# Optimization experiments

Measured on AMD Instinct MI355X. Metric: run time of the kernel, lower is better.

The kernel has to match this reference:

```python
import jax, jax.numpy as jnp
import numpy as np

CIN, COUT, R, N, B = 4, 4, 4, 4096, 32

def setup_inputs() -> dict:
    key = jax.random.key(0)
    k1, k2, k3 = jax.random.split(key, 3)
    x = jax.random.normal(k1, (CIN, B, N), dtype=jnp.float32)
    # torch.nn.init.normal(std=0.01)
    G = 0.01 * jax.random.normal(k2, (CIN, COUT, R, N), dtype=jnp.float32)
    H = 0.01 * jax.random.normal(k3, (CIN, COUT, R, N), dtype=jnp.float32)
    return {"x": x, "G": G, "H": H}

def reference(x, G, H):
    """LDR layer, displacement='toep_corner' (cycle=True).

    For each channel pair (i,j):
        M_ij = sum_s C_1(G[i,j,s]) @ C_{-1}(H[i,j,s])^T
    where C_f(v) is the f-circulant matrix with first column v
    (= Krylov matrix of the f-unit-circulant shift Z_f with vector v).
    out[j] = sum_i M_ij @ x[i]^T  (batched over batch dim).

    Identities used (F = DFT):
      C_1(u) y      = ifft(fft(u) * fft(y))
      C_1(u)^T y    = fft(fft(u) * ifft(y))
      C_f(v)        = D^{-1} C_1(D v) D,  D = diag(zeta^k), zeta = f^{1/n}
      => C_{-1}(h)^T y = D * fft(fft(D*h) * ifft(conj(D)*y)), D_k = exp(i*pi*k/n)
    All channel pairs and ranks are batched in a single FFT call (no Python
    loops over channels, unlike the original double loop).
    """
    cin, b, n = x.shape
    k = jnp.arange(n)
    D = jnp.exp(1j * jnp.pi * k / n).astype(jnp.complex64)   # zeta^k for f=-1
    Dinv = jnp.conj(D)

    # --- step 1: t[i,j,s,b,:] = C_{-1}(H[i,j,s])^T x[i,b,:]  -> (cin,cout,r,b,n)
    Hf = jnp.fft.fft(D * H.astype(jnp.complex64), axis=-1)           # (cin,cout,r,n)
    Xf = jnp.fft.ifft(Dinv * x.astype(jnp.complex64), axis=-1)       # (cin,b,n)
    t = D * jnp.fft.fft(Hf[:, :, :, None, :] * Xf[:, None, None, :, :], axis=-1)

    # --- step 2: out[j,b,:] = Re ifft( sum_{i,s} fft(G[i,j,s]) * fft(t[i,j,s,b]) )
    Gf = jnp.fft.fft(G, axis=-1).astype(jnp.complex64)               # (cin,cout,r,n)
    Tf = jnp.fft.fft(t, axis=-1)                                     # (cin,cout,r,b,n)
    Yf = jnp.einsum('ijsn,ijsbn->jbn', Gf, Tf)                       # (cout,b,n)
    return jnp.real(jnp.fft.ifft(Yf, axis=-1)).astype(x.dtype)
```

## Files before the change

kernel.cpp:

```cpp
#include <hip/hip_runtime.h>
#include <math.h>


#define NFFT  4096
#define NT    256
#define CIN   4
#define COUT  4
#define RANK  4
#define BATCH 32
#define PI_F  3.14159265358979323846f

__device__ __forceinline__ float2 cmul(float2 a, float2 b) {
    return make_float2(a.x*b.x - a.y*b.y, a.x*b.y + a.y*b.x);
}
__device__ __forceinline__ float2 cadd(float2 a, float2 b){ return make_float2(a.x+b.x, a.y+b.y); }
__device__ __forceinline__ float2 csub(float2 a, float2 b){ return make_float2(a.x-b.x, a.y-b.y); }

__device__ __forceinline__ int SW(int e){ return e ^ ((e >> 4) & 15); }

template<int SIGN>
__device__ __forceinline__ void dft16(float2 v[16]) {
    const float sgn = (float)SIGN;
    const float C8 = 0.923879532511287f, S8 = 0.382683432365090f, H2 = 0.707106781186548f;
    const float2 w1 = make_float2( C8,  sgn*S8);
    const float2 w2 = make_float2( H2,  sgn*H2);
    const float2 w3 = make_float2( S8,  sgn*C8);
    const float2 w4 = make_float2(0.f,  sgn);
    const float2 w6 = make_float2(-H2,  sgn*H2);
    const float2 w9 = make_float2(-C8, -sgn*S8);
    float2 t[16];
    #pragma unroll
    for (int p = 0; p < 4; ++p) {
        float2 a0 = v[p], a1 = v[p+4], a2 = v[p+8], a3 = v[p+12];
        float2 b0 = cadd(a0,a2), b1 = csub(a0,a2), b2 = cadd(a1,a3), b3 = csub(a1,a3);
        float2 ib3 = make_float2(-sgn*b3.y, sgn*b3.x);
        float2 X0 = cadd(b0,b2), X2c = csub(b0,b2);
        float2 X1 = cadd(b1,ib3), X3 = csub(b1,ib3);
        if (p == 1) { X1 = cmul(X1,w1); X2c = cmul(X2c,w2); X3 = cmul(X3,w3); }
        else if (p == 2) { X1 = cmul(X1,w2); X2c = cmul(X2c,w4); X3 = cmul(X3,w6); }
        else if (p == 3) { X1 = cmul(X1,w3); X2c = cmul(X2c,w6); X3 = cmul(X3,w9); }
        t[4*p+0]=X0; t[4*p+1]=X1; t[4*p+2]=X2c; t[4*p+3]=X3;
    }
    #pragma unroll
    for (int q = 0; q < 4; ++q) {
        float2 a0 = t[q], a1 = t[q+4], a2 = t[q+8], a3 = t[q+12];
        float2 b0 = cadd(a0,a2), b1 = csub(a0,a2), b2 = cadd(a1,a3), b3 = csub(a1,a3);
        float2 ib3 = make_float2(-sgn*b3.y, sgn*b3.x);
        v[q+0]  = cadd(b0,b2);
        v[q+8]  = csub(b0,b2);
        v[q+4]  = cadd(b1,ib3);
        v[q+12] = csub(b1,ib3);
    }
}

__device__ __forceinline__ void twiddle16(float2 v[16], float ang) {
    float sn, cs; __sincosf(ang, &sn, &cs);
    float2 w = make_float2(cs, sn), t = w;
    v[1] = cmul(v[1], t);
    #pragma unroll
    for (int k = 2; k < 16; ++k) { t = cmul(t, w); v[k] = cmul(v[k], t); }
}

template<int SIGN>
__device__ void fft4096_r16(float2 v[16], float2* lds, int tid) {
    dft16<SIGN>(v);
    twiddle16(v, (float)SIGN * 2.0f * PI_F * (float)tid / 4096.0f);
    #pragma unroll
    for (int k = 0; k < 16; ++k) lds[SW(16*tid + k)] = v[k];
    __syncthreads();
    #pragma unroll
    for (int r = 0; r < 16; ++r) v[r] = lds[SW(tid + 256*r)];
    dft16<SIGN>(v);
    twiddle16(v, (float)SIGN * 2.0f * PI_F * (float)(tid >> 4) / 256.0f);
    __syncthreads();
    {
        const int q = tid & 15, p = tid >> 4;
        #pragma unroll
        for (int k = 0; k < 16; ++k) lds[SW(q + 256*p + 16*k)] = v[k];
    }
    __syncthreads();
    #pragma unroll
    for (int r = 0; r < 16; ++r) v[r] = lds[SW(tid + 256*r)];
    dft16<SIGN>(v);
    __syncthreads();
}

__global__ __launch_bounds__(NT, 2) void ldr_pre_k(
    const float* __restrict__ x, const float* __restrict__ G, const float* __restrict__ H,
    float2* __restrict__ Hf, float2* __restrict__ Gf, float2* __restrict__ Xf)
{
    __shared__ float2 lds[NFFT];
    const int tid = threadIdx.x;
    const int bid = blockIdx.x;
    float2 v[16];
    if (bid < 64) {
        const float* h = H + (size_t)bid * NFFT;
        float sn, cs; __sincosf(PI_F * (float)tid / (float)NFFT, &sn, &cs);
        float2 d = make_float2(cs, sn);
        const float2 dstep = make_float2(0.980785280403230449f, 0.195090322016128268f);
        #pragma unroll
        for (int k = 0; k < 16; ++k) {
            float hv = h[tid + 256*k];
            v[k] = make_float2(d.x*hv, d.y*hv);
            d = cmul(d, dstep);
        }
        fft4096_r16<-1>(v, lds, tid);
        float2* o = Hf + (size_t)bid * NFFT;
        #pragma unroll
        for (int k = 0; k < 16; ++k) o[tid + 256*k] = v[k];
    } else if (bid < 128) {
        const int row = bid - 64;
        const float* g = G + (size_t)row * NFFT;
        #pragma unroll
        for (int k = 0; k < 16; ++k) v[k] = make_float2(g[tid + 256*k], 0.0f);
        fft4096_r16<-1>(v, lds, tid);
        float2* o = Gf + (size_t)row * NFFT;
        #pragma unroll
        for (int k = 0; k < 16; ++k) o[tid + 256*k] = v[k];
    } else {
        const int row = bid - 128;
        const float* xp = x + (size_t)row * NFFT;
        float sn, cs; __sincosf(PI_F * (float)tid / (float)NFFT, &sn, &cs);
        float2 d = make_float2(cs, -sn);
        const float2 dstep = make_float2(0.980785280403230449f, -0.195090322016128268f);
        #pragma unroll
        for (int k = 0; k < 16; ++k) {
            float xv = xp[tid + 256*k];
            v[k] = make_float2(d.x*xv, d.y*xv);
            d = cmul(d, dstep);
        }
        fft4096_r16<1>(v, lds, tid);
        const float invn = 1.0f / (float)NFFT;
        float2* o = Xf + (size_t)row * NFFT;
        #pragma unroll
        for (int k = 0; k < 16; ++k) o[tid + 256*k] = make_float2(v[k].x*invn, v[k].y*invn);
    }
}

__global__ __launch_bounds__(NT, 2) void ldr_mid_k(
    const float2* __restrict__ Hf, const float2* __restrict__ Xf,
    const float2* __restrict__ Gf, float2* __restrict__ Ph)
{
    __shared__ float2 lds[NFFT];
    const int tid = threadIdx.x;
    const int bid = blockIdx.x;
    const int b   = bid & (BATCH - 1);
    const int is_ = bid >> 5;
    const int s   = is_ & 3;
    const int ij  = is_ >> 2;
    const int i   = ij >> 2;
    const int j   = ij & 3;
    const float2* xrow = Xf + (size_t)(i*BATCH + b) * NFFT;
    const float2* hrow = Hf + (size_t)is_ * NFFT;
    const float2* grow = Gf + (size_t)is_ * NFFT;

    float2 v[16];
    #pragma unroll
    for (int k = 0; k < 16; ++k) {
        const int e = tid + 256*k;
        v[k] = cmul(hrow[e], xrow[e]);
    }
    fft4096_r16<-1>(v, lds, tid);
    {
        float sn, cs; __sincosf(PI_F * (float)tid / (float)NFFT, &sn, &cs);
        float2 d = make_float2(cs, sn);
        const float2 dstep = make_float2(0.980785280403230449f, 0.195090322016128268f);
        #pragma unroll
        for (int k = 0; k < 16; ++k) { v[k] = cmul(v[k], d); d = cmul(d, dstep); }
    }
    fft4096_r16<-1>(v, lds, tid);
    const int u = i * RANK + s;
    float2* prow = Ph + (size_t)((u*COUT + j)*BATCH + b) * (NFFT/2);
    float2 y0 = cmul(grow[tid], v[0]);
    if (tid == 0) {
        const float2 ynyq = cmul(grow[2048], v[8]);
        y0 = make_float2(y0.x, ynyq.x);
    }
    prow[tid] = y0;
    #pragma unroll
    for (int k = 1; k < 8; ++k) {
        const int e = tid + 256*k;
        prow[e] = cmul(grow[e], v[k]);
    }
}

__global__ __launch_bounds__(NT, 2) void ldr_fin_k(
    const float2* __restrict__ Ph, float* __restrict__ out)
{
    __shared__ float2 lds[NFFT];
    __shared__ float2 sh[NFFT/2];
    const int tid = threadIdx.x;
    const int bid = blockIdx.x;
    const int b = bid & (BATCH - 1);
    const int j = bid >> 5;

    float2 a[8];
    #pragma unroll
    for (int k = 0; k < 8; ++k) a[k] = make_float2(0.0f, 0.0f);
    #pragma unroll
    for (int u = 0; u < 16; ++u) {
        const float2* row = Ph + (size_t)((u*COUT + j)*BATCH + b) * (NFFT/2);
        #pragma unroll
        for (int k = 0; k < 8; ++k) a[k] = cadd(a[k], row[tid + 256*k]);
    }
    #pragma unroll
    for (int k = 0; k < 8; ++k) sh[tid + 256*k] = a[k];
    __syncthreads();

    const float dc  = sh[0].x;
    const float nyq = sh[0].y;
    float2 v[16];
    #pragma unroll
    for (int k = 0; k < 8; ++k) v[k] = a[k];
    if (tid == 0) v[0] = make_float2(dc, 0.0f);
    #pragma unroll
    for (int k = 8; k < 16; ++k) {
        const int m = 4096 - (tid + 256*k);
        if (m == 2048) {
            v[k] = make_float2(nyq, 0.0f);
        } else {
            float2 c = sh[m];
            v[k] = make_float2(c.x, -c.y);
        }
    }
    fft4096_r16<1>(v, lds, tid);
    const float invn = 1.0f / (float)NFFT;
    float* orow = out + (size_t)bid * NFFT;
    #pragma unroll
    for (int k = 0; k < 16; ++k) orow[tid + 256*k] = v[k].x * invn;
}

extern "C" void kernel_launch(void* const* d_in, const int* in_sizes, int n_in,
                              void* d_out, int out_size, void* d_ws, size_t ws_size,
                              hipStream_t stream) {
    const float* x = (const float*)d_in[0];
    const float* G = (const float*)d_in[1];
    const float* H = (const float*)d_in[2];
    float* out = (float*)d_out;

    float2* Hf = (float2*)d_ws;
    float2* Gf = Hf + (size_t)64 * NFFT;
    float2* Xf = Gf + (size_t)64 * NFFT;
    float2* Ph = Xf + (size_t)128 * NFFT;

    ldr_pre_k<<<256, NT, 0, stream>>>(x, G, H, Hf, Gf, Xf);
    ldr_mid_k<<<CIN * COUT * RANK * BATCH, NT, 0, stream>>>(Hf, Xf, Gf, Ph);
    ldr_fin_k<<<COUT * BATCH, NT, 0, stream>>>(Ph, out);
}
```

Before: 108.4 us.

## Fuse rank pairs in mid kernel, prune second forward FFT outputs, vectorize reduction

The mid kernel now processes two ranks per block and accumulates their G-weighted spectra in registers, halving the Ph partial-sum buffer and the blocks launched. The second forward FFT uses a pruned final radix-16 stage that computes only the lower half of the outputs the real-output path needs. The final reduction reads half as many partial rows with float4 loads. Twiddle generation is split into odd and even chains to shorten the serial dependency. In exchange each mid block does twice the work, giving fewer blocks and less parallelism.

```diff
diff --git a/kernel.cpp b/kernel.cpp
--- a/kernel.cpp
+++ b/kernel.cpp
@@ -53,12 +53,53 @@
     }
 }
 
+template<int SIGN>
+__device__ __forceinline__ void dft16_low(float2 v[16]) {
+    const float sgn = (float)SIGN;
+    const float C8 = 0.923879532511287f, S8 = 0.382683432365090f, H2 = 0.707106781186548f;
+    const float2 w1 = make_float2( C8,  sgn*S8);
+    const float2 w2 = make_float2( H2,  sgn*H2);
+    const float2 w3 = make_float2( S8,  sgn*C8);
+    const float2 w4 = make_float2(0.f,  sgn);
+    const float2 w6 = make_float2(-H2,  sgn*H2);
+    const float2 w9 = make_float2(-C8, -sgn*S8);
+    float2 t[16];
+    #pragma unroll
+    for (int p = 0; p < 4; ++p) {
+        float2 a0 = v[p], a1 = v[p+4], a2 = v[p+8], a3 = v[p+12];
+        float2 b0 = cadd(a0,a2), b1 = csub(a0,a2), b2 = cadd(a1,a3), b3 = csub(a1,a3);
+        float2 ib3 = make_float2(-sgn*b3.y, sgn*b3.x);
+        float2 X0 = cadd(b0,b2), X2c = csub(b0,b2);
+        float2 X1 = cadd(b1,ib3), X3 = csub(b1,ib3);
+        if (p == 1) { X1 = cmul(X1,w1); X2c = cmul(X2c,w2); X3 = cmul(X3,w3); }
+        else if (p == 2) { X1 = cmul(X1,w2); X2c = cmul(X2c,w4); X3 = cmul(X3,w6); }
+        else if (p == 3) { X1 = cmul(X1,w3); X2c = cmul(X2c,w6); X3 = cmul(X3,w9); }
+        t[4*p+0]=X0; t[4*p+1]=X1; t[4*p+2]=X2c; t[4*p+3]=X3;
+    }
+    #pragma unroll
+    for (int q = 0; q < 4; ++q) {
+        float2 a0 = t[q], a1 = t[q+4], a2 = t[q+8], a3 = t[q+12];
+        float2 b0 = cadd(a0,a2), b1 = csub(a0,a2), b2 = cadd(a1,a3), b3 = csub(a1,a3);
+        float2 ib3 = make_float2(-sgn*b3.y, sgn*b3.x);
+        v[q+0]  = cadd(b0,b2);
+        v[q+4]  = cadd(b1,ib3);
+        if (q == 0) v[8] = csub(b0,b2);
+    }
+}
+
 __device__ __forceinline__ void twiddle16(float2 v[16], float ang) {
     float sn, cs; __sincosf(ang, &sn, &cs);
-    float2 w = make_float2(cs, sn), t = w;
-    v[1] = cmul(v[1], t);
-    #pragma unroll
-    for (int k = 2; k < 16; ++k) { t = cmul(t, w); v[k] = cmul(v[k], t); }
+    float2 w  = make_float2(cs, sn);
+    float2 w2 = cmul(w, w);
+    float2 to = w;
+    float2 te = w2;
+    v[1] = cmul(v[1], to);
+    v[2] = cmul(v[2], te);
+    #pragma unroll
+    for (int k = 3; k < 16; k += 2) {
+        to = cmul(to, w2); v[k] = cmul(v[k], to);
+        if (k + 1 < 16) { te = cmul(te, w2); v[k+1] = cmul(v[k+1], te); }
+    }
 }
 
 template<int SIGN>
@@ -83,6 +124,30 @@
     for (int r = 0; r < 16; ++r) v[r] = lds[SW(tid + 256*r)];
     dft16<SIGN>(v);
     __syncthreads();
+}
+
+template<bool TAIL_SYNC>
+__device__ void fft4096_fwd_low(float2 v[16], float2* lds, int tid) {
+    dft16<-1>(v);
+    twiddle16(v, -2.0f * PI_F * (float)tid / 4096.0f);
+    #pragma unroll
+    for (int k = 0; k < 16; ++k) lds[SW(16*tid + k)] = v[k];
+    __syncthreads();
+    #pragma unroll
+    for (int r = 0; r < 16; ++r) v[r] = lds[SW(tid + 256*r)];
+    dft16<-1>(v);
+    twiddle16(v, -2.0f * PI_F * (float)(tid >> 4) / 256.0f);
+    __syncthreads();
+    {
+        const int q = tid & 15, p = tid >> 4;
+        #pragma unroll
+        for (int k = 0; k < 16; ++k) lds[SW(q + 256*p + 16*k)] = v[k];
+    }
+    __syncthreads();
+    #pragma unroll
+    for (int r = 0; r < 16; ++r) v[r] = lds[SW(tid + 256*r)];
+    dft16_low<-1>(v);
+    if (TAIL_SYNC) __syncthreads();
 }
 
 __global__ __launch_bounds__(NT, 2) void ldr_pre_k(
@@ -145,43 +210,54 @@
     const int tid = threadIdx.x;
     const int bid = blockIdx.x;
     const int b   = bid & (BATCH - 1);
-    const int is_ = bid >> 5;
-    const int s   = is_ & 3;
-    const int ij  = is_ >> 2;
+    const int is2 = bid >> 5;
+    const int sg  = is2 & 1;
+    const int ij  = is2 >> 1;
     const int i   = ij >> 2;
     const int j   = ij & 3;
     const float2* xrow = Xf + (size_t)(i*BATCH + b) * NFFT;
-    const float2* hrow = Hf + (size_t)is_ * NFFT;
-    const float2* grow = Gf + (size_t)is_ * NFFT;
-
-    float2 v[16];
-    #pragma unroll
-    for (int k = 0; k < 16; ++k) {
-        const int e = tid + 256*k;
-        v[k] = cmul(hrow[e], xrow[e]);
-    }
-    fft4096_r16<-1>(v, lds, tid);
-    {
-        float sn, cs; __sincosf(PI_F * (float)tid / (float)NFFT, &sn, &cs);
-        float2 d = make_float2(cs, sn);
-        const float2 dstep = make_float2(0.980785280403230449f, 0.195090322016128268f);
-        #pragma unroll
-        for (int k = 0; k < 16; ++k) { v[k] = cmul(v[k], d); d = cmul(d, dstep); }
-    }
-    fft4096_r16<-1>(v, lds, tid);
-    const int u = i * RANK + s;
+
+    float2 acc[8];
+    float  accNyq = 0.0f;
+    #pragma unroll
+    for (int k = 0; k < 8; ++k) acc[k] = make_float2(0.0f, 0.0f);
+
+    #pragma unroll
+    for (int ss = 0; ss < 2; ++ss) {
+        const int row = ij*RANK + sg*2 + ss;
+        const float2* hrow = Hf + (size_t)row * NFFT;
+        const float2* grow = Gf + (size_t)row * NFFT;
+        float2 v[16];
+        #pragma unroll
+        for (int k = 0; k < 16; ++k) {
+            const int e = tid + 256*k;
+            v[k] = cmul(hrow[e], xrow[e]);
+        }
+        fft4096_r16<-1>(v, lds, tid);
+        {
+            float sn, cs; __sincosf(PI_F * (float)tid / (float)NFFT, &sn, &cs);
+            float2 d = make_float2(cs, sn);
+            const float2 dstep = make_float2(0.980785280403230449f, 0.195090322016128268f);
+            #pragma unroll
+            for (int k = 0; k < 16; ++k) { v[k] = cmul(v[k], d); d = cmul(d, dstep); }
+        }
+        if (ss == 0) fft4096_fwd_low<true >(v, lds, tid);
+        else         fft4096_fwd_low<false>(v, lds, tid);
+        #pragma unroll
+        for (int k = 0; k < 8; ++k) {
+            const int e = tid + 256*k;
+            acc[k] = cadd(acc[k], cmul(grow[e], v[k]));
+        }
+        accNyq += cmul(grow[2048], v[8]).x;
+    }
+
+    const int u = i*2 + sg;
     float2* prow = Ph + (size_t)((u*COUT + j)*BATCH + b) * (NFFT/2);
-    float2 y0 = cmul(grow[tid], v[0]);
-    if (tid == 0) {
-        const float2 ynyq = cmul(grow[2048], v[8]);
-        y0 = make_float2(y0.x, ynyq.x);
-    }
+    float2 y0 = acc[0];
+    if (tid == 0) y0 = make_float2(acc[0].x, accNyq);
     prow[tid] = y0;
     #pragma unroll
-    for (int k = 1; k < 8; ++k) {
-        const int e = tid + 256*k;
-        prow[e] = cmul(grow[e], v[k]);
-    }
+    for (int k = 1; k < 8; ++k) prow[tid + 256*k] = acc[k];
 }
 
 __global__ __launch_bounds__(NT, 2) void ldr_fin_k(
@@ -194,24 +270,28 @@
     const int b = bid & (BATCH - 1);
     const int j = bid >> 5;
 
-    float2 a[8];
-    #pragma unroll
-    for (int k = 0; k < 8; ++k) a[k] = make_float2(0.0f, 0.0f);
-    #pragma unroll
-    for (int u = 0; u < 16; ++u) {
-        const float2* row = Ph + (size_t)((u*COUT + j)*BATCH + b) * (NFFT/2);
-        #pragma unroll
-        for (int k = 0; k < 8; ++k) a[k] = cadd(a[k], row[tid + 256*k]);
-    }
-    #pragma unroll
-    for (int k = 0; k < 8; ++k) sh[tid + 256*k] = a[k];
+    float4 a4[4];
+    #pragma unroll
+    for (int k = 0; k < 4; ++k) a4[k] = make_float4(0.f, 0.f, 0.f, 0.f);
+    #pragma unroll
+    for (int u = 0; u < 8; ++u) {
+        const float4* row4 = (const float4*)(Ph + (size_t)((u*COUT + j)*BATCH + b) * (NFFT/2));
+        #pragma unroll
+        for (int k = 0; k < 4; ++k) {
+            float4 t = row4[tid + 256*k];
+            a4[k].x += t.x; a4[k].y += t.y; a4[k].z += t.z; a4[k].w += t.w;
+        }
+    }
+    float4* sh4 = (float4*)sh;
+    #pragma unroll
+    for (int k = 0; k < 4; ++k) sh4[tid + 256*k] = a4[k];
     __syncthreads();
 
     const float dc  = sh[0].x;
     const float nyq = sh[0].y;
     float2 v[16];
     #pragma unroll
-    for (int k = 0; k < 8; ++k) v[k] = a[k];
+    for (int k = 0; k < 8; ++k) v[k] = sh[tid + 256*k];
     if (tid == 0) v[0] = make_float2(dc, 0.0f);
     #pragma unroll
     for (int k = 8; k < 16; ++k) {
@@ -244,6 +324,6 @@
     float2* Ph = Xf + (size_t)128 * NFFT;
 
     ldr_pre_k<<<256, NT, 0, stream>>>(x, G, H, Hf, Gf, Xf);
-    ldr_mid_k<<<CIN * COUT * RANK * BATCH, NT, 0, stream>>>(Hf, Xf, Gf, Ph);
+    ldr_mid_k<<<CIN * COUT * RANK * BATCH / 2, NT, 0, stream>>>(Hf, Xf, Gf, Ph);
     ldr_fin_k<<<COUT * BATCH, NT, 0, stream>>>(Ph, out);
 }
```

Result: slower. 135.4 us (+24.9%).

## Pack two ranks per complex FFT and store partial spectra in half precision

Applied to the files above, without the earlier changes.

The middle kernel now handles two rank terms per block, packing them as the real and imaginary parts of a single complex FFT. This works because the t sequences for real inputs are real, so one FFT pass covers both. The two spectra are separated with Hermitian symmetry through LDS, which halves the grid and the number of FFTs. Partial products are stored as half2, and the final reduction reads them with 128-bit loads, halving intermediate memory traffic at the cost of fp16 precision in the accumulated spectra. The twiddle recurrence is also split into even and odd chains to shorten the dependency chain.

```diff
diff --git a/kernel.cpp b/kernel.cpp
--- a/kernel.cpp
+++ b/kernel.cpp
@@ -1,4 +1,5 @@
 #include <hip/hip_runtime.h>
+#include <hip/hip_fp16.h>
 #include <math.h>
 
 
@@ -55,10 +56,17 @@
 
 __device__ __forceinline__ void twiddle16(float2 v[16], float ang) {
     float sn, cs; __sincosf(ang, &sn, &cs);
-    float2 w = make_float2(cs, sn), t = w;
-    v[1] = cmul(v[1], t);
-    #pragma unroll
-    for (int k = 2; k < 16; ++k) { t = cmul(t, w); v[k] = cmul(v[k], t); }
+    float2 w  = make_float2(cs, sn);
+    float2 w2 = cmul(w, w);
+    float2 to = w;
+    float2 te = w2;
+    v[1] = cmul(v[1], to);
+    v[2] = cmul(v[2], te);
+    #pragma unroll
+    for (int k = 3; k < 16; k += 2) {
+        to = cmul(to, w2); v[k] = cmul(v[k], to);
+        if (k + 1 < 16) { te = cmul(te, w2); v[k+1] = cmul(v[k+1], te); }
+    }
 }
 
 template<int SIGN>
@@ -139,26 +147,32 @@
 
 __global__ __launch_bounds__(NT, 2) void ldr_mid_k(
     const float2* __restrict__ Hf, const float2* __restrict__ Xf,
-    const float2* __restrict__ Gf, float2* __restrict__ Ph)
+    const float2* __restrict__ Gf, __half2* __restrict__ Ph)
 {
     __shared__ float2 lds[NFFT];
     const int tid = threadIdx.x;
     const int bid = blockIdx.x;
     const int b   = bid & (BATCH - 1);
-    const int is_ = bid >> 5;
-    const int s   = is_ & 3;
-    const int ij  = is_ >> 2;
+    const int ip  = bid >> 5;
+    const int pr  = ip & 1;
+    const int ij  = ip >> 1;
     const int i   = ij >> 2;
     const int j   = ij & 3;
+    const int r0  = ij*RANK + 2*pr;
     const float2* xrow = Xf + (size_t)(i*BATCH + b) * NFFT;
-    const float2* hrow = Hf + (size_t)is_ * NFFT;
-    const float2* grow = Gf + (size_t)is_ * NFFT;
+    const float2* h0 = Hf + (size_t)r0 * NFFT;
+    const float2* h1 = h0 + NFFT;
+    const float2* g0 = Gf + (size_t)r0 * NFFT;
+    const float2* g1 = g0 + NFFT;
 
     float2 v[16];
     #pragma unroll
     for (int k = 0; k < 16; ++k) {
         const int e = tid + 256*k;
-        v[k] = cmul(hrow[e], xrow[e]);
+        const float2 xv = xrow[e];
+        const float2 a  = cmul(h0[e], xv);
+        const float2 c  = cmul(h1[e], xv);
+        v[k] = make_float2(a.x - c.y, a.y + c.x);
     }
     fft4096_r16<-1>(v, lds, tid);
     {
@@ -169,23 +183,34 @@
         for (int k = 0; k < 16; ++k) { v[k] = cmul(v[k], d); d = cmul(d, dstep); }
     }
     fft4096_r16<-1>(v, lds, tid);
-    const int u = i * RANK + s;
-    float2* prow = Ph + (size_t)((u*COUT + j)*BATCH + b) * (NFFT/2);
-    float2 y0 = cmul(grow[tid], v[0]);
-    if (tid == 0) {
-        const float2 ynyq = cmul(grow[2048], v[8]);
-        y0 = make_float2(y0.x, ynyq.x);
-    }
-    prow[tid] = y0;
-    #pragma unroll
-    for (int k = 1; k < 8; ++k) {
+
+    #pragma unroll
+    for (int k = 8; k < 16; ++k) lds[SW(tid + 256*k)] = v[k];
+    __syncthreads();
+
+    const int u = i*2 + pr;
+    __half2* prow = Ph + (size_t)((u*COUT + j)*BATCH + b) * (NFFT/2);
+    #pragma unroll
+    for (int k = 0; k < 8; ++k) {
         const int e = tid + 256*k;
-        prow[e] = cmul(grow[e], v[k]);
+        const float2 Zk = v[k];
+        float2 Zm;
+        if (e == 0) Zm = Zk;
+        else        Zm = lds[SW(4096 - e)];
+        const float2 V1 = make_float2(0.5f*(Zk.x + Zm.x), 0.5f*(Zk.y - Zm.y));
+        const float2 V2 = make_float2(0.5f*(Zk.y + Zm.y), 0.5f*(Zm.x - Zk.x));
+        float2 Y = cadd(cmul(g0[e], V1), cmul(g1[e], V2));
+        if (k == 0 && tid == 0) {
+            const float2 Zn = v[8];
+            const float Ynyq = g0[2048].x * Zn.x + g1[2048].x * Zn.y;
+            Y = make_float2(Y.x, Ynyq);
+        }
+        prow[e] = __floats2half2_rn(Y.x, Y.y);
     }
 }
 
 __global__ __launch_bounds__(NT, 2) void ldr_fin_k(
-    const float2* __restrict__ Ph, float* __restrict__ out)
+    const __half2* __restrict__ Ph, float* __restrict__ out)
 {
     __shared__ float2 lds[NFFT];
     __shared__ float2 sh[NFFT/2];
@@ -196,22 +221,35 @@
 
     float2 a[8];
     #pragma unroll
-    for (int k = 0; k < 8; ++k) a[k] = make_float2(0.0f, 0.0f);
-    #pragma unroll
-    for (int u = 0; u < 16; ++u) {
-        const float2* row = Ph + (size_t)((u*COUT + j)*BATCH + b) * (NFFT/2);
-        #pragma unroll
-        for (int k = 0; k < 8; ++k) a[k] = cadd(a[k], row[tid + 256*k]);
-    }
-    #pragma unroll
-    for (int k = 0; k < 8; ++k) sh[tid + 256*k] = a[k];
+    for (int k = 0; k < 8; ++k) a[k] = make_float2(0.f, 0.f);
+    #pragma unroll
+    for (int u = 0; u < 8; ++u) {
+        const int4* row4 = (const int4*)(Ph + (size_t)((u*COUT + j)*BATCH + b) * (NFFT/2));
+        #pragma unroll
+        for (int c = 0; c < 2; ++c) {
+            const int4 w = row4[tid + 256*c];
+            const int ww[4] = { w.x, w.y, w.z, w.w };
+            #pragma unroll
+            for (int r = 0; r < 4; ++r) {
+                __half2 h = *(const __half2*)&ww[r];
+                float2 f = __half22float2(h);
+                a[c*4+r] = cadd(a[c*4+r], f);
+            }
+        }
+    }
+    float4* sh4 = (float4*)sh;
+    #pragma unroll
+    for (int c = 0; c < 2; ++c) {
+        sh4[2*(tid + 256*c) + 0] = make_float4(a[c*4+0].x, a[c*4+0].y, a[c*4+1].x, a[c*4+1].y);
+        sh4[2*(tid + 256*c) + 1] = make_float4(a[c*4+2].x, a[c*4+2].y, a[c*4+3].x, a[c*4+3].y);
+    }
     __syncthreads();
 
     const float dc  = sh[0].x;
     const float nyq = sh[0].y;
     float2 v[16];
     #pragma unroll
-    for (int k = 0; k < 8; ++k) v[k] = a[k];
+    for (int k = 0; k < 8; ++k) v[k] = sh[tid + 256*k];
     if (tid == 0) v[0] = make_float2(dc, 0.0f);
     #pragma unroll
     for (int k = 8; k < 16; ++k) {
@@ -238,12 +276,12 @@
     const float* H = (const float*)d_in[2];
     float* out = (float*)d_out;
 
-    float2* Hf = (float2*)d_ws;
-    float2* Gf = Hf + (size_t)64 * NFFT;
-    float2* Xf = Gf + (size_t)64 * NFFT;
-    float2* Ph = Xf + (size_t)128 * NFFT;
+    float2*  Hf = (float2*)d_ws;
+    float2*  Gf = Hf + (size_t)64 * NFFT;
+    float2*  Xf = Gf + (size_t)64 * NFFT;
+    __half2* Ph = (__half2*)(Xf + (size_t)128 * NFFT);
 
     ldr_pre_k<<<256, NT, 0, stream>>>(x, G, H, Hf, Gf, Xf);
-    ldr_mid_k<<<CIN * COUT * RANK * BATCH, NT, 0, stream>>>(Hf, Xf, Gf, Ph);
+    ldr_mid_k<<<CIN * COUT * RANK * BATCH / 2, NT, 0, stream>>>(Hf, Xf, Gf, Ph);
     ldr_fin_k<<<COUT * BATCH, NT, 0, stream>>>(Ph, out);
 }
```

Measured after the change: 91.21 us. -15.9%, faster.
